# Kernel tuning notes

Measured on AMD Instinct MI355X. Metric: run time of the kernel, lower is better.

## Reference

```python
import jax, jax.numpy as jnp
import numpy as np

B, C, R = 8, 256, 14
H_HEADS = 4
KD = 16            # key_dim
D_V = 64           # attn_ratio * key_dim
KS = 5             # dw conv kernel
N = R * R * R      # tokens


def _bias_idx():
    # replicate original offset logic: only first two coords (|dx|,|dy|) used
    pts = np.array(np.meshgrid(np.arange(R), np.arange(R), np.arange(R), indexing='ij'))
    pts = pts.reshape(3, -1).T  # (N, 3) in itertools.product order
    dx = np.abs(pts[:, 0:1] - pts[None, :, 0])  # (N, N)
    dy = np.abs(pts[:, 1:2] - pts[None, :, 1])
    return (dx * R + dy).astype(np.int32)  # (N, N), values in [0, R*R)


def setup_inputs() -> dict:
    key = jax.random.key(0)
    ks = jax.random.split(key, 12)
    cph = C // H_HEADS
    qkv_out = 2 * KD + D_V
    inp = {
        'x': jax.random.normal(ks[0], (B, C, R, R, R), jnp.float32),
        'Wqkv': jax.random.normal(ks[1], (H_HEADS, qkv_out, cph), jnp.float32) * 0.05,
        'qkv_scale': 1.0 + 0.05 * jax.random.normal(ks[2], (H_HEADS, qkv_out), jnp.float32),
        'qkv_bias': 0.05 * jax.random.normal(ks[3], (H_HEADS, qkv_out), jnp.float32),
        'Wdw': jax.random.normal(ks[4], (H_HEADS, KD, 1, KS, KS, KS), jnp.float32) * 0.05,
        'dw_scale': 1.0 + 0.05 * jax.random.normal(ks[5], (H_HEADS, KD), jnp.float32),
        'dw_bias': 0.05 * jax.random.normal(ks[6], (H_HEADS, KD), jnp.float32),
        'Wproj': jax.random.normal(ks[7], (C, D_V * H_HEADS), jnp.float32) * 0.02,
        'proj_scale': 1.0 + 0.05 * jax.random.normal(ks[8], (C,), jnp.float32),
        'proj_bias': 0.05 * jax.random.normal(ks[9], (C,), jnp.float32),
        'attention_biases': 0.02 * jax.random.normal(ks[10], (H_HEADS, R * R), jnp.float32),
        'bias_idx': jnp.asarray(_bias_idx()),
    }
    return inp


def reference(x, Wqkv, qkv_scale, qkv_bias, Wdw, dw_scale, dw_bias,
              Wproj, proj_scale, proj_bias, attention_biases, bias_idx):
    scale = KD ** (-0.5)
    ab = attention_biases[:, bias_idx]  # (h, N, N) relative-position bias gather
    feats_in = jnp.split(x, H_HEADS, axis=1)  # h x (B, C/h, R, R, R)
    dn = ('NCDHW', 'OIDHW', 'NCDHW')
    feats_out = []
    feat = feats_in[0]
    for i in range(H_HEADS):
        if i > 0:
            feat = feat + feats_in[i]
        # 1x1x1 conv QKV + fused BN (inference-style scale/shift)
        y = jnp.einsum('oc,bcxyz->boxyz', Wqkv[i], feat)
        y = y * qkv_scale[i][:, None, None, None] + qkv_bias[i][:, None, None, None]
        q = y[:, :KD]
        k = y[:, KD:2 * KD]
        v = y[:, 2 * KD:]
        # depthwise conv on q + fused BN
        q = jax.lax.conv_general_dilated(q, Wdw[i], (1, 1, 1), 'SAME',
                                         feature_group_count=KD, dimension_numbers=dn)
        q = q * dw_scale[i][:, None, None, None] + dw_bias[i][:, None, None, None]
        qf = q.reshape(B, KD, N)
        kf = k.reshape(B, KD, N)
        vf = v.reshape(B, D_V, N)
        attn = jnp.einsum('bcn,bcm->bnm', qf, kf) * scale + ab[i]  # (B, N, N)
        attn = jax.nn.softmax(attn, axis=-1)
        feat = jnp.einsum('bcm,bnm->bcn', vf, attn).reshape(B, D_V, R, R, R)
        feats_out.append(feat)
    h = jax.nn.relu(jnp.concatenate(feats_out, axis=1))  # (B, d*h, R, R, R)
    out = jnp.einsum('oc,bcxyz->boxyz', Wproj, h)
    out = out * proj_scale[:, None, None, None] + proj_bias[:, None, None, None]
    return out
```

## Files before the change

kernel.cpp:

```cpp
#include <hip/hip_runtime.h>

#define B_    8
#define C_    256
#define R_    14
#define R2    196
#define N3    2744
#define NP    2752
#define NH    4
#define KD    16
#define DV    64
#define QKVO  96
#define MT    64
#define NTILE 43
#define SPLIT 4
#define TPC   11

#define SC2   0.36067376f
#define LOG2E 1.44269504f
#define ABSZ  406

typedef __attribute__((ext_vector_type(8))) short short8v;
typedef __attribute__((ext_vector_type(4))) short short4v;
typedef __attribute__((ext_vector_type(4))) float float4v;

__device__ __forceinline__ int iabs(int v){ return v < 0 ? -v : v; }

__device__ __forceinline__ short f2bf(float f){
    union { float f; unsigned int u; } c; c.f = f;
    return (short)((c.u + 0x7FFFu + ((c.u >> 16) & 1u)) >> 16);
}
__device__ __forceinline__ float bf2f(short s){
    union { unsigned int u; float f; } c; c.u = ((unsigned int)(unsigned short)s) << 16;
    return c.f;
}

__global__ __launch_bounds__(256)
void wprep_kernel(const float* __restrict__ Wp, short* __restrict__ whi,
                  short* __restrict__ wlo, const float* __restrict__ Wqkv,
                  const float* __restrict__ qsc, short* __restrict__ wqhi,
                  short* __restrict__ wqlo)
{
    int i = blockIdx.x * 256 + threadIdx.x;
    {
        float w = Wp[i];
        short hi = f2bf(w);
        short lo = f2bf(w - bf2f(hi));
        whi[i] = hi; wlo[i] = lo;
    }
    if (i < NH * QKVO * 64) {
        int o_all = i >> 6;
        float w = Wqkv[i] * qsc[o_all];
        short hi = f2bf(w);
        short lo = f2bf(w - bf2f(hi));
        wqhi[i] = hi; wqlo[i] = lo;
    }
}

__global__ __launch_bounds__(256, 2)
void qkv_mfma(const float* __restrict__ x, float* __restrict__ h,
              const float* __restrict__ pacc, const float* __restrict__ pl,
              const short* __restrict__ wqhi, const short* __restrict__ wqlo,
              const float* __restrict__ qbi,
              float* __restrict__ q0, short* __restrict__ kbf, short* __restrict__ vbf,
              int head)
{
    __shared__ short fhi[64][72];
    __shared__ short flo[64][72];
    __shared__ float bsh[96];
    __shared__ float linv_s[64];

    const int b = blockIdx.y;
    const int n0 = blockIdx.x * 64;
    const int t = threadIdx.x;
    const int w = t >> 6, l = t & 63, g = l >> 4, ln = l & 15;

    if (t < 96) bsh[t] = qbi[head * QKVO + t];

    if (head > 0) {
        if (t < 64) {
            int n = n0 + t;
            float lt = pl[(size_t)(b * SPLIT + 0) * NP + n]
                     + pl[(size_t)(b * SPLIT + 1) * NP + n]
                     + pl[(size_t)(b * SPLIT + 2) * NP + n]
                     + pl[(size_t)(b * SPLIT + 3) * NP + n];
            linv_s[t] = 1.f / lt;
        }
        __syncthreads();
    }

    {
        const int sc_ = t & 63;
        const int sng = (t >> 6) * 16;
        const int nb = n0 + sng;
        const float* xs = x + ((size_t)b * C_ + head * DV + sc_) * N3 + nb;
        float fv[16];
        const bool fullblk = (nb + 15 < N3);
        if (fullblk) {
#pragma unroll
            for (int e4 = 0; e4 < 4; e4++) {
                float4 xv = ((const float4*)xs)[e4];
                fv[4*e4+0] = xv.x; fv[4*e4+1] = xv.y; fv[4*e4+2] = xv.z; fv[4*e4+3] = xv.w;
            }
        } else {
#pragma unroll
            for (int e = 0; e < 16; e++) fv[e] = (nb + e < N3) ? xs[e] : 0.f;
        }
        if (head > 0) {
            const float* pb = pacc + (size_t)b * SPLIT * DV * NP + (size_t)sc_ * NP + nb;
            float* hw = h + ((size_t)b * C_ + (head - 1) * DV + sc_) * N3 + nb;
            const size_t zs = (size_t)DV * NP;
            if (fullblk) {
#pragma unroll
                for (int e4 = 0; e4 < 4; e4++) {
                    float4 a0 = ((const float4*)(pb         ))[e4];
                    float4 a1 = ((const float4*)(pb +     zs))[e4];
                    float4 a2 = ((const float4*)(pb + 2 * zs))[e4];
                    float4 a3 = ((const float4*)(pb + 3 * zs))[e4];
                    float hc[4];
                    hc[0] = (a0.x + a1.x + a2.x + a3.x) * linv_s[sng + 4*e4 + 0];
                    hc[1] = (a0.y + a1.y + a2.y + a3.y) * linv_s[sng + 4*e4 + 1];
                    hc[2] = (a0.z + a1.z + a2.z + a3.z) * linv_s[sng + 4*e4 + 2];
                    hc[3] = (a0.w + a1.w + a2.w + a3.w) * linv_s[sng + 4*e4 + 3];
                    *(float4*)&hw[4*e4] = make_float4(hc[0], hc[1], hc[2], hc[3]);
                    fv[4*e4+0] += hc[0]; fv[4*e4+1] += hc[1];
                    fv[4*e4+2] += hc[2]; fv[4*e4+3] += hc[3];
                }
            } else {
#pragma unroll
                for (int e = 0; e < 16; e++) {
                    if (nb + e < N3) {
                        float a = pb[e] + pb[e + zs] + pb[e + 2*zs] + pb[e + 3*zs];
                        float hc = a * linv_s[sng + e];
                        hw[e] = hc;
                        fv[e] += hc;
                    }
                }
            }
        }
#pragma unroll
        for (int e = 0; e < 16; e++) {
            short hi = f2bf(fv[e]);
            short lo = f2bf(fv[e] - bf2f(hi));
            fhi[sng + e][sc_] = hi;
            flo[sng + e][sc_] = lo;
        }
    }
    __syncthreads();

    float4v acc[6];
#pragma unroll
    for (int os = 0; os < 6; os++) acc[os] = (float4v){0.f, 0.f, 0.f, 0.f};

    const short* wqh = wqhi + head * QKVO * 64;
    const short* wql = wqlo + head * QKVO * 64;
#pragma unroll
    for (int ck = 0; ck < 2; ck++) {
        short8v bh = *(const short8v*)&fhi[w * 16 + ln][ck * 32 + g * 8];
        short8v bl = *(const short8v*)&flo[w * 16 + ln][ck * 32 + g * 8];
#pragma unroll
        for (int os = 0; os < 6; os++) {
            size_t off = (size_t)(os * 16 + ln) * 64 + ck * 32 + g * 8;
            short8v wh = *(const short8v*)(wqh + off);
            short8v wl = *(const short8v*)(wql + off);
            acc[os] = __builtin_amdgcn_mfma_f32_16x16x32_bf16(wh, bh, acc[os], 0, 0, 0);
            acc[os] = __builtin_amdgcn_mfma_f32_16x16x32_bf16(wh, bl, acc[os], 0, 0, 0);
            acc[os] = __builtin_amdgcn_mfma_f32_16x16x32_bf16(wl, bh, acc[os], 0, 0, 0);
        }
    }

    const int n_ = n0 + w * 16 + ln;
    const bool ok = n_ < N3;
    float* qo = q0 + (size_t)b * KD * NP;
    short* ko = kbf + (size_t)b * NP * 16 + (size_t)n_ * 16;
    short* vo = vbf + (size_t)b * DV * NP;
#pragma unroll
    for (int os = 0; os < 6; os++) {
#pragma unroll
        for (int r = 0; r < 4; r++) {
            int o = os * 16 + g * 4 + r;
            float y = ok ? acc[os][r] + bsh[o] : 0.f;
            if (o < KD)            qo[(size_t)o * NP + n_] = y;
            else if (o < 2 * KD)   ko[o - KD] = f2bf(y);
            else                   vo[(size_t)(o - 2 * KD) * NP + n_] = f2bf(y);
        }
    }
}

__global__ __launch_bounds__(256)
void dwconv_kernel(float* __restrict__ q0, const float* __restrict__ Wdw,
                   const float* __restrict__ dsc, const float* __restrict__ dbi,
                   int head)
{
    __shared__ float pv[18 * 18 * 18];
    int b = blockIdx.y, c = blockIdx.x;
    int t = threadIdx.x;
    float* qc = q0 + ((size_t)b * KD + c) * NP;

    for (int i = t; i < 5832; i += 256) pv[i] = 0.f;
    __syncthreads();
    for (int i = t; i < N3; i += 256) {
        int xx = i / R2; int rem = i - xx * R2; int yy = rem / R_; int zz = rem - yy * R_;
        pv[(xx + 2) * 324 + (yy + 2) * 18 + (zz + 2)] = qc[i];
    }
    __syncthreads();

    const float* w = Wdw + (head * KD + c) * 125;
    float scl = dsc[head * KD + c], bia = dbi[head * KD + c];

    if (t < R2) {
        int x = t / R_, y = t - (t / R_) * R_;
        float acc[14];
#pragma unroll
        for (int z = 0; z < 14; z++) acc[z] = 0.f;
#pragma unroll
        for (int a = 0; a < 5; a++) {
#pragma unroll
            for (int bb = 0; bb < 5; bb++) {
                const float* base = &pv[(x + a) * 324 + (y + bb) * 18];
                float col[18];
#pragma unroll
                for (int j = 0; j < 18; j++) col[j] = base[j];
#pragma unroll
                for (int cc = 0; cc < 5; cc++) {
                    float wv = w[a * 25 + bb * 5 + cc];
#pragma unroll
                    for (int z = 0; z < 14; z++) acc[z] += wv * col[z + cc];
                }
            }
        }
        float* qo = qc + x * R2 + y * R_;
#pragma unroll
        for (int z = 0; z < 14; z++) qo[z] = acc[z] * scl + bia;
    }
}

__global__ __launch_bounds__(256, 4)
void attn_partial(const float* __restrict__ q0, const short* __restrict__ kbf,
                  const short* __restrict__ vbf, float* __restrict__ pacc,
                  float* __restrict__ pl, const float* __restrict__ abias, int head)
{
    __shared__ short ktT[64][40];
    __shared__ short vtT[64][72];
    __shared__ short plds[4][16][72];
    __shared__ int   mxa[64];
    __shared__ float ab2[ABSZ];

    const int b = blockIdx.y, z = blockIdx.z;
    const int qbase = blockIdx.x * 64;
    const int t = threadIdx.x;
    const int w = t >> 6;
    const int l = t & 63;
    const int g = l >> 4;
    const int ln = l & 15;

    for (int i = t; i < ABSZ; i += 256)
        ab2[i] = (i < 196) ? abias[head * R2 + i] * LOG2E : -20000.0f;

    const float* qq  = q0  + (size_t)b * KD * NP;
    const short* kbs = kbf + (size_t)b * NP * 16;
    const short* vbs = vbf + (size_t)b * DV * NP;

    {
        int mm = t & 63, dg = t >> 6;
        short4v zz = {0, 0, 0, 0};
        *(short4v*)&ktT[mm][16 + dg * 4] = zz;
    }

    const int n_my = qbase + w * 16 + ln;
    short8v qf;
#pragma unroll
    for (int j = 0; j < 8; j++) {
        int d = g * 8 + j;
        qf[j] = (d < KD) ? f2bf(qq[(size_t)d * NP + n_my]) : (short)0;
    }
    const int nmc = n_my < N3 ? n_my : 0;
    const int nx = nmc / R2, ny = (nmc - nx * R2) / R_;

    float4v acc[4];
#pragma unroll
    for (int cs = 0; cs < 4; cs++) acc[cs] = (float4v){0.f, 0.f, 0.f, 0.f};
    float lsum = 0.f;

    const int tEnd = min(z * TPC + TPC, NTILE);
    for (int t0 = z * TPC; t0 < tEnd; t0++) {
        const int m0 = t0 * MT;
        __syncthreads();
        {
            int mm = t >> 2, kq = t & 3;
            short4v kv = *(const short4v*)(kbs + (size_t)(m0 + mm) * 16 + kq * 4);
            *(short4v*)&ktT[mm][kq * 4] = kv;
        }
        {
            int c = t >> 2, mq = t & 3;
            const short* vs = vbs + (size_t)c * NP + m0 + mq * 16;
            short8v s0 = ((const short8v*)vs)[0];
            short8v s1 = ((const short8v*)vs)[1];
            *(short8v*)&vtT[c][mq * 16]     = s0;
            *(short8v*)&vtT[c][mq * 16 + 8] = s1;
        }
        if (t < 64) {
            int m = m0 + t;
            int mx, my;
            if (m < N3) { mx = m / R2; int rem = m - mx * R2; my = rem / R_; }
            else        { mx = 27; my = 27; }
            mxa[t] = (mx << 8) | my;
        }
        __syncthreads();

#pragma unroll
        for (int ms = 0; ms < 4; ms++) {
            short8v af = *(const short8v*)&ktT[ms * 16 + ln][g * 8];
            float4v zf = {0.f, 0.f, 0.f, 0.f};
            float4v s = __builtin_amdgcn_mfma_f32_16x16x32_bf16(af, qf, zf, 0, 0, 0);
            int4 pk4 = *(const int4*)&mxa[ms * 16 + g * 4];
            int pka[4] = {pk4.x, pk4.y, pk4.z, pk4.w};
            float p[4];
#pragma unroll
            for (int r = 0; r < 4; r++) {
                int mx = pka[r] >> 8, my = pka[r] & 255;
                int dx, idx;
                asm("v_sad_u32 %0, %1, %2, 0" : "=v"(dx) : "v"(nx), "v"(mx));
                int t14 = dx * 14;
                asm("v_sad_u32 %0, %1, %2, %3" : "=v"(idx) : "v"(ny), "v"(my), "v"(t14));
                float lg2 = fmaf(s[r], SC2, ab2[idx]);
                p[r] = exp2f(lg2);
                lsum += p[r];
            }
            unsigned pk01, pk23;
            asm("v_cvt_pk_bf16_f32 %0, %1, %2" : "=v"(pk01) : "v"(p[0]), "v"(p[1]));
            asm("v_cvt_pk_bf16_f32 %0, %1, %2" : "=v"(pk23) : "v"(p[2]), "v"(p[3]));
            uint2 pw = make_uint2(pk01, pk23);
            *(uint2*)&plds[w][ln][ms * 16 + g * 4] = pw;
        }

#pragma unroll
        for (int ck = 0; ck < 2; ck++) {
            short8v pa = *(const short8v*)&plds[w][ln][ck * 32 + g * 8];
#pragma unroll
            for (int cs = 0; cs < 4; cs++) {
                short8v vf = *(const short8v*)&vtT[cs * 16 + ln][ck * 32 + g * 8];
                acc[cs] = __builtin_amdgcn_mfma_f32_16x16x32_bf16(pa, vf, acc[cs], 0, 0, 0);
            }
        }
    }

    lsum += __shfl_xor(lsum, 16);
    lsum += __shfl_xor(lsum, 32);

    float* pbase = pacc + (size_t)(b * SPLIT + z) * DV * NP;
    if (l < 16) {
        int n_l = qbase + w * 16 + l;
        if (n_l < N3) pl[(size_t)(b * SPLIT + z) * NP + n_l] = lsum;
    }
    const int n0w = qbase + w * 16 + g * 4;
    if (n0w < N3) {
#pragma unroll
        for (int cs = 0; cs < 4; cs++) {
            int c = cs * 16 + ln;
            *(float4v*)&pbase[(size_t)c * NP + n0w] = acc[cs];
        }
    }
}

__global__ __launch_bounds__(256)
void attn_combine(const float* __restrict__ pacc, const float* __restrict__ pl,
                  float* __restrict__ h, int head)
{
    int b = blockIdx.y;
    int ch0 = blockIdx.z * 16;
    int r = blockIdx.x * 256 + threadIdx.x;
    if (r >= N3) return;
    float l = 0.f;
#pragma unroll
    for (int z = 0; z < SPLIT; z++) l += pl[(size_t)(b * SPLIT + z) * NP + r];
    float inv = 1.f / l;
    float* hb = h + ((size_t)b * C_ + head * DV) * N3 + r;
    const float* pb = pacc + (size_t)b * SPLIT * DV * NP + r;
#pragma unroll
    for (int cc = 0; cc < 16; cc++) {
        int ch = ch0 + cc;
        float a = 0.f;
#pragma unroll
        for (int z = 0; z < SPLIT; z++) a += pb[(size_t)(z * DV + ch) * NP];
        hb[(size_t)ch * N3] = a * inv;
    }
}

__global__ __launch_bounds__(256, 2)
void proj_kernel(const float* __restrict__ h, const short* __restrict__ whi,
                 const short* __restrict__ wlo, const float* __restrict__ psc,
                 const float* __restrict__ pbi, float* __restrict__ out)
{
    __shared__ short hhi[64][40];
    __shared__ short hlo[64][40];

    const int b = blockIdx.y;
    const int n0 = blockIdx.x * 64;
    const int t = threadIdx.x;
    const int w = t >> 6, l = t & 63, g = l >> 4, ln = l & 15;

    float4v acc[4][4];
#pragma unroll
    for (int os = 0; os < 4; os++)
#pragma unroll
        for (int ns = 0; ns < 4; ns++) acc[os][ns] = (float4v){0.f, 0.f, 0.f, 0.f};

    const float* hb = h + (size_t)b * C_ * N3;
    const int sc = t >> 3;
    const int sn = (t & 7) * 8;

    for (int c0 = 0; c0 < 256; c0 += 32) {
        __syncthreads();
        {
            const float* hsrc = hb + (size_t)(c0 + sc) * N3 + n0 + sn;
            float4 f0 = ((const float4*)hsrc)[0];
            float4 f1 = ((const float4*)hsrc)[1];
            float va[8] = { f0.x, f0.y, f0.z, f0.w, f1.x, f1.y, f1.z, f1.w };
#pragma unroll
            for (int u = 0; u < 8; u++) {
                float v = va[u] > 0.f ? va[u] : 0.f;
                short hi = f2bf(v);
                short lo = f2bf(v - bf2f(hi));
                hhi[sn + u][sc] = hi;
                hlo[sn + u][sc] = lo;
            }
        }
        __syncthreads();

        short8v wh[4], wl[4];
#pragma unroll
        for (int os = 0; os < 4; os++) {
            size_t off = (size_t)(64 * w + os * 16 + ln) * 256 + c0 + g * 8;
            wh[os] = *(const short8v*)(whi + off);
            wl[os] = *(const short8v*)(wlo + off);
        }
#pragma unroll
        for (int ns = 0; ns < 4; ns++) {
            short8v bh = *(const short8v*)&hhi[ns * 16 + ln][g * 8];
            short8v bl = *(const short8v*)&hlo[ns * 16 + ln][g * 8];
#pragma unroll
            for (int os = 0; os < 4; os++) {
                acc[os][ns] = __builtin_amdgcn_mfma_f32_16x16x32_bf16(wh[os], bh, acc[os][ns], 0, 0, 0);
                acc[os][ns] = __builtin_amdgcn_mfma_f32_16x16x32_bf16(wh[os], bl, acc[os][ns], 0, 0, 0);
                acc[os][ns] = __builtin_amdgcn_mfma_f32_16x16x32_bf16(wl[os], bh, acc[os][ns], 0, 0, 0);
            }
        }
    }

    float* ob = out + (size_t)b * C_ * N3;
#pragma unroll
    for (int os = 0; os < 4; os++) {
#pragma unroll
        for (int r = 0; r < 4; r++) {
            int o = 64 * w + os * 16 + g * 4 + r;
            float s0 = psc[o], b0 = pbi[o];
#pragma unroll
            for (int ns = 0; ns < 4; ns++) {
                int n = n0 + ns * 16 + ln;
                if (n < N3) ob[(size_t)o * N3 + n] = acc[os][ns][r] * s0 + b0;
            }
        }
    }
}

extern "C" void kernel_launch(void* const* d_in, const int* in_sizes, int n_in,
                              void* d_out, int out_size, void* d_ws, size_t ws_size,
                              hipStream_t stream)
{
    const float* x    = (const float*)d_in[0];
    const float* Wqkv = (const float*)d_in[1];
    const float* qsc  = (const float*)d_in[2];
    const float* qbi  = (const float*)d_in[3];
    const float* Wdw  = (const float*)d_in[4];
    const float* dsc  = (const float*)d_in[5];
    const float* dbi  = (const float*)d_in[6];
    const float* Wp   = (const float*)d_in[7];
    const float* psc  = (const float*)d_in[8];
    const float* pbi  = (const float*)d_in[9];
    const float* ab   = (const float*)d_in[10];

    float* out = (float*)d_out;
    char*  wsb = (char*)d_ws;
    float* q0   = (float*)wsb;
    short* kbf  = (short*)(q0 + (size_t)B_ * KD * NP);
    short* vbf  = kbf + (size_t)B_ * NP * 16;
    float* h    = (float*)(vbf + (size_t)B_ * DV * NP);
    float* pacc = h + (size_t)B_ * C_ * N3;
    float* pl   = pacc + (size_t)B_ * SPLIT * DV * NP;
    short* whi  = (short*)(pl + (size_t)B_ * SPLIT * NP);
    short* wlo  = whi + 256 * 256;
    short* wqhi = wlo + 256 * 256;
    short* wqlo = wqhi + NH * QKVO * 64;

    wprep_kernel<<<256, 256, 0, stream>>>(Wp, whi, wlo, Wqkv, qsc, wqhi, wqlo);

    for (int head = 0; head < NH; head++) {
        qkv_mfma<<<dim3(43, B_), 256, 0, stream>>>(x, h, pacc, pl, wqhi, wqlo, qbi,
                                                   q0, kbf, vbf, head);
        dwconv_kernel<<<dim3(KD, B_), 256, 0, stream>>>(q0, Wdw, dsc, dbi, head);
        attn_partial<<<dim3(43, B_, SPLIT), 256, 0, stream>>>(q0, kbf, vbf, pacc, pl, ab, head);
    }
    attn_combine<<<dim3(11, B_, 4), 256, 0, stream>>>(pacc, pl, h, NH - 1);
    proj_kernel<<<dim3(43, B_), 256, 0, stream>>>(h, whi, wlo, psc, pbi, out);
}
```

Measured before the change: 341.0 us.

## Prefetch next K/V tile into registers and fuse final attention combine into projection

The attention loop now loads the next K/V tile from global memory into registers while the current tile is being computed, which hides global load latency behind the MFMA work. The separate attn_combine launch for the last head is removed. Instead, proj_kernel reduces the four split partial accumulators and normalizes them by the summed softmax denominators when it stages channels 192-255. This saves one kernel launch and one write and read of that head's output. The cost is extra register pressure in attn_partial and four times the memory reads for those channels inside proj_kernel.

```diff
diff --git a/kernel.cpp b/kernel.cpp
--- a/kernel.cpp
+++ b/kernel.cpp
@@ -281,29 +281,37 @@
     for (int cs = 0; cs < 4; cs++) acc[cs] = (float4v){0.f, 0.f, 0.f, 0.f};
     float lsum = 0.f;
 
+    const int smm = t >> 2, sq = t & 3;
+    short4v kpre;
+    short8v vpre0, vpre1;
+    {
+        const int m0 = (z * TPC) * MT;
+        kpre = *(const short4v*)(kbs + (size_t)(m0 + smm) * 16 + sq * 4);
+        const short* vs = vbs + (size_t)smm * NP + m0 + sq * 16;
+        vpre0 = ((const short8v*)vs)[0];
+        vpre1 = ((const short8v*)vs)[1];
+    }
+
     const int tEnd = min(z * TPC + TPC, NTILE);
     for (int t0 = z * TPC; t0 < tEnd; t0++) {
         const int m0 = t0 * MT;
         __syncthreads();
-        {
-            int mm = t >> 2, kq = t & 3;
-            short4v kv = *(const short4v*)(kbs + (size_t)(m0 + mm) * 16 + kq * 4);
-            *(short4v*)&ktT[mm][kq * 4] = kv;
-        }
-        {
-            int c = t >> 2, mq = t & 3;
-            const short* vs = vbs + (size_t)c * NP + m0 + mq * 16;
-            short8v s0 = ((const short8v*)vs)[0];
-            short8v s1 = ((const short8v*)vs)[1];
-            *(short8v*)&vtT[c][mq * 16]     = s0;
-            *(short8v*)&vtT[c][mq * 16 + 8] = s1;
-        }
+        *(short4v*)&ktT[smm][sq * 4]      = kpre;
+        *(short8v*)&vtT[smm][sq * 16]     = vpre0;
+        *(short8v*)&vtT[smm][sq * 16 + 8] = vpre1;
         if (t < 64) {
             int m = m0 + t;
             int mx, my;
             if (m < N3) { mx = m / R2; int rem = m - mx * R2; my = rem / R_; }
             else        { mx = 27; my = 27; }
             mxa[t] = (mx << 8) | my;
+        }
+        if (t0 + 1 < tEnd) {
+            const int m1 = (t0 + 1) * MT;
+            kpre = *(const short4v*)(kbs + (size_t)(m1 + smm) * 16 + sq * 4);
+            const short* vs = vbs + (size_t)smm * NP + m1 + sq * 16;
+            vpre0 = ((const short8v*)vs)[0];
+            vpre1 = ((const short8v*)vs)[1];
         }
         __syncthreads();
 
@@ -362,43 +370,30 @@
     }
 }
 
-__global__ __launch_bounds__(256)
-void attn_combine(const float* __restrict__ pacc, const float* __restrict__ pl,
-                  float* __restrict__ h, int head)
-{
-    int b = blockIdx.y;
-    int ch0 = blockIdx.z * 16;
-    int r = blockIdx.x * 256 + threadIdx.x;
-    if (r >= N3) return;
-    float l = 0.f;
-#pragma unroll
-    for (int z = 0; z < SPLIT; z++) l += pl[(size_t)(b * SPLIT + z) * NP + r];
-    float inv = 1.f / l;
-    float* hb = h + ((size_t)b * C_ + head * DV) * N3 + r;
-    const float* pb = pacc + (size_t)b * SPLIT * DV * NP + r;
-#pragma unroll
-    for (int cc = 0; cc < 16; cc++) {
-        int ch = ch0 + cc;
-        float a = 0.f;
-#pragma unroll
-        for (int z = 0; z < SPLIT; z++) a += pb[(size_t)(z * DV + ch) * NP];
-        hb[(size_t)ch * N3] = a * inv;
-    }
-}
-
 __global__ __launch_bounds__(256, 2)
-void proj_kernel(const float* __restrict__ h, const short* __restrict__ whi,
+void proj_kernel(const float* __restrict__ h, const float* __restrict__ pacc,
+                 const float* __restrict__ pl, const short* __restrict__ whi,
                  const short* __restrict__ wlo, const float* __restrict__ psc,
                  const float* __restrict__ pbi, float* __restrict__ out)
 {
     __shared__ short hhi[64][40];
     __shared__ short hlo[64][40];
+    __shared__ float linv_s[64];
 
     const int b = blockIdx.y;
     const int n0 = blockIdx.x * 64;
     const int t = threadIdx.x;
     const int w = t >> 6, l = t & 63, g = l >> 4, ln = l & 15;
 
+    if (t < 64) {
+        int n = n0 + t;
+        float lt = pl[(size_t)(b * SPLIT + 0) * NP + n]
+                 + pl[(size_t)(b * SPLIT + 1) * NP + n]
+                 + pl[(size_t)(b * SPLIT + 2) * NP + n]
+                 + pl[(size_t)(b * SPLIT + 3) * NP + n];
+        linv_s[t] = 1.f / lt;
+    }
+
     float4v acc[4][4];
 #pragma unroll
     for (int os = 0; os < 4; os++)
@@ -411,11 +406,39 @@
 
     for (int c0 = 0; c0 < 256; c0 += 32) {
         __syncthreads();
-        {
+        if (c0 < 192) {
             const float* hsrc = hb + (size_t)(c0 + sc) * N3 + n0 + sn;
             float4 f0 = ((const float4*)hsrc)[0];
             float4 f1 = ((const float4*)hsrc)[1];
             float va[8] = { f0.x, f0.y, f0.z, f0.w, f1.x, f1.y, f1.z, f1.w };
+#pragma unroll
+            for (int u = 0; u < 8; u++) {
+                float v = va[u] > 0.f ? va[u] : 0.f;
+                short hi = f2bf(v);
+                short lo = f2bf(v - bf2f(hi));
+                hhi[sn + u][sc] = hi;
+                hlo[sn + u][sc] = lo;
+            }
+        } else {
+            const int cl = c0 + sc - 192;
+            const int nb = n0 + sn;
+            const bool in = nb < N3;
+            float va[8] = {0,0,0,0,0,0,0,0};
+            if (in) {
+                const float* pb = pacc + (size_t)b * SPLIT * DV * NP + (size_t)cl * NP + nb;
+                const size_t zs = (size_t)DV * NP;
+#pragma unroll
+                for (int e4 = 0; e4 < 2; e4++) {
+                    float4 a0 = ((const float4*)(pb         ))[e4];
+                    float4 a1 = ((const float4*)(pb +     zs))[e4];
+                    float4 a2 = ((const float4*)(pb + 2 * zs))[e4];
+                    float4 a3 = ((const float4*)(pb + 3 * zs))[e4];
+                    va[4*e4+0] = (a0.x + a1.x + a2.x + a3.x) * linv_s[sn + 4*e4 + 0];
+                    va[4*e4+1] = (a0.y + a1.y + a2.y + a3.y) * linv_s[sn + 4*e4 + 1];
+                    va[4*e4+2] = (a0.z + a1.z + a2.z + a3.z) * linv_s[sn + 4*e4 + 2];
+                    va[4*e4+3] = (a0.w + a1.w + a2.w + a3.w) * linv_s[sn + 4*e4 + 3];
+                }
+            }
 #pragma unroll
             for (int u = 0; u < 8; u++) {
                 float v = va[u] > 0.f ? va[u] : 0.f;
@@ -500,6 +523,5 @@
         dwconv_kernel<<<dim3(KD, B_), 256, 0, stream>>>(q0, Wdw, dsc, dbi, head);
         attn_partial<<<dim3(43, B_, SPLIT), 256, 0, stream>>>(q0, kbf, vbf, pacc, pl, ab, head);
     }
-    attn_combine<<<dim3(11, B_, 4), 256, 0, stream>>>(pacc, pl, h, NH - 1);
-    proj_kernel<<<dim3(43, B_), 256, 0, stream>>>(h, whi, wlo, psc, pbi, out);
-}
+    proj_kernel<<<dim3(43, B_), 256, 0, stream>>>(h, pacc, pl, whi, wlo, psc, pbi, out);
+}
```

Result: no change. 337.6 us (-1.0%).
